# Kernel tuning notes

Measured on AMD Instinct MI355X. Metric: run time of the kernel, lower is better.

The kernel has to match this reference:

```python
import jax, jax.numpy as jnp
import numpy as np

N_NODES = 50000
N_EDGES = 800000
H = 128
LN_EPS = 1e-5


def setup_inputs() -> dict:
    key = jax.random.key(0)
    ks = jax.random.split(key, 8)
    x = jax.random.normal(ks[0], (N_NODES, H), dtype=jnp.float32)
    senders = jax.random.randint(ks[1], (N_EDGES,), 0, N_NODES, dtype=jnp.int32)
    receivers = jax.random.randint(ks[2], (N_EDGES,), 0, N_NODES, dtype=jnp.int32)
    edge_feat = jax.random.normal(ks[3], (N_EDGES, H), dtype=jnp.float32)
    # message_proj1: Linear(3H, H) -- PyTorch-style init scale
    lim = 1.0 / np.sqrt(3 * H)
    W1 = jax.random.uniform(ks[4], (3 * H, H), minval=-lim, maxval=lim, dtype=jnp.float32)
    b1 = jax.random.uniform(ks[5], (H,), minval=-lim, maxval=lim, dtype=jnp.float32)
    ln_gamma = jnp.ones((H,), dtype=jnp.float32)
    ln_beta = jnp.zeros((H,), dtype=jnp.float32)
    return {"x": x, "senders": senders, "receivers": receivers, "edge_feat": edge_feat,
            "W1": W1, "b1": b1, "ln_gamma": ln_gamma, "ln_beta": ln_beta}


def _layernorm(h, gamma, beta):
    mu = jnp.mean(h, axis=-1, keepdims=True)
    var = jnp.mean(jnp.square(h - mu), axis=-1, keepdims=True)
    return gamma * (h - mu) * jax.lax.rsqrt(var + LN_EPS) + beta


def reference(x, senders, receivers, edge_feat, W1, b1, ln_gamma, ln_beta):
    # gather sender/receiver node states, concat with edge features: [E, 3H]
    cat = jnp.concatenate((x[senders], x[receivers], edge_feat), axis=-1)
    msg = jax.nn.relu(cat @ W1 + b1)                      # [E, H]
    aggr = jax.ops.segment_sum(msg, receivers, num_segments=x.shape[0])  # [N, H]
    h = aggr + x                                          # residual
    return _layernorm(h, ln_gamma, ln_beta)
```

## Files before the change

### kernel.cpp

```cpp
#include <hip/hip_runtime.h>

#define NN 50000
#define NE 800000
#define H 128
#define K3H 384

typedef __bf16 bf16x8 __attribute__((ext_vector_type(8)));
typedef float f32x4 __attribute__((ext_vector_type(4)));

__device__ inline unsigned short f2bf(float f) {
    unsigned int u = __float_as_uint(f);
    u += 0x7FFFu + ((u >> 16) & 1u);
    return (unsigned short)(u >> 16);
}

__global__ void zero_aggr(float4* aggr) {
    int i = blockIdx.x * blockDim.x + threadIdx.x;
    aggr[i] = make_float4(0.f, 0.f, 0.f, 0.f);
}

__global__ void w1_transpose(const float* __restrict__ W1, unsigned short* __restrict__ W1t) {
    int o = blockIdx.x * 256 + threadIdx.x;
    if (o < K3H * H) {
        int n = o / K3H;
        int k = o - n * K3H;
        W1t[o] = f2bf(W1[k * H + n]);
    }
}

__global__ __launch_bounds__(256) void edge_gemm(
        const float* __restrict__ x,
        const int* __restrict__ senders,
        const int* __restrict__ receivers,
        const float* __restrict__ edge_feat,
        const unsigned short* __restrict__ W1t,
        const float* __restrict__ b1,
        float* __restrict__ aggr) {
    __shared__ short lds_a[128 * 72];
    __shared__ short lds_b[128 * 72];
    __shared__ int s_send[128];
    __shared__ int s_recv[128];

    const int tid = threadIdx.x;
    const int e0 = blockIdx.x * 128;

    if (tid < 128) s_send[tid] = senders[e0 + tid];
    else           s_recv[tid - 128] = receivers[e0 + tid - 128];
    __syncthreads();

    const int lane = tid & 63;
    const int wave = tid >> 6;
    const int wm = wave >> 1, wn = wave & 1;
    const int q = lane >> 4, l15 = lane & 15;

    f32x4 acc[4][4];
#pragma unroll
    for (int i = 0; i < 4; i++)
#pragma unroll
        for (int j = 0; j < 4; j++) acc[i][j] = (f32x4){0.f, 0.f, 0.f, 0.f};

    const int a_seg  = tid & 15;
    const int a_row0 = tid >> 4;
    const int b_seg  = tid & 7;
    const int b_row0 = tid >> 3;

    for (int c = 0; c < 6; ++c) {
        const int coloff = (c & 1) * 64;
#pragma unroll
        for (int p = 0; p < 8; ++p) {
            int row = a_row0 + p * 16;
            const float* src;
            if (c < 2)      src = x + (size_t)s_send[row] * H + coloff;
            else if (c < 4) src = x + (size_t)s_recv[row] * H + coloff;
            else            src = edge_feat + (size_t)(e0 + row) * H + coloff;
            float4 v = *(const float4*)(src + a_seg * 4);
            uint2 pk;
            pk.x = (unsigned)f2bf(v.x) | ((unsigned)f2bf(v.y) << 16);
            pk.y = (unsigned)f2bf(v.z) | ((unsigned)f2bf(v.w) << 16);
            *(uint2*)&lds_a[row * 72 + a_seg * 4] = pk;
        }
#pragma unroll
        for (int p = 0; p < 4; ++p) {
            int n = b_row0 + p * 32;
            uint4 v = *(const uint4*)(W1t + n * K3H + c * 64 + b_seg * 8);
            *(uint4*)&lds_b[n * 72 + b_seg * 8] = v;
        }
        __syncthreads();

        const short* pa = lds_a + (wm * 64 + l15) * 72 + q * 8;
        const short* pb = lds_b + (wn * 64 + l15) * 72 + q * 8;
#pragma unroll
        for (int ks = 0; ks < 2; ++ks) {
            bf16x8 af[4], bfr[4];
#pragma unroll
            for (int mi = 0; mi < 4; mi++)
                af[mi] = *(const bf16x8*)(const void*)(pa + mi * 16 * 72 + ks * 32);
#pragma unroll
            for (int ni = 0; ni < 4; ni++)
                bfr[ni] = *(const bf16x8*)(const void*)(pb + ni * 16 * 72 + ks * 32);
#pragma unroll
            for (int mi = 0; mi < 4; mi++)
#pragma unroll
                for (int ni = 0; ni < 4; ni++)
                    acc[mi][ni] = __builtin_amdgcn_mfma_f32_16x16x32_bf16(
                        af[mi], bfr[ni], acc[mi][ni], 0, 0, 0);
        }
        __syncthreads();
    }

    float bias[4];
#pragma unroll
    for (int ni = 0; ni < 4; ni++) bias[ni] = b1[wn * 64 + ni * 16 + l15];

#pragma unroll
    for (int mi = 0; mi < 4; mi++) {
        int rbase = wm * 64 + mi * 16 + q * 4;
#pragma unroll
        for (int r = 0; r < 4; r++) {
            int rl = rbase + r;
            int recv = s_recv[rl];
            float* dst = aggr + (size_t)recv * H + wn * 64 + l15;
#pragma unroll
            for (int ni = 0; ni < 4; ni++) {
                float v = acc[mi][ni][r] + bias[ni];
                if (v > 0.f) atomicAdd(dst + ni * 16, v);
            }
        }
    }
}

__global__ void residual_ln(const float* __restrict__ aggr, const float* __restrict__ x,
                            const float* __restrict__ gamma, const float* __restrict__ beta,
                            float* __restrict__ out) {
    int node = blockIdx.x * 4 + (threadIdx.x >> 6);
    int lane = threadIdx.x & 63;
    size_t off = (size_t)node * H + lane * 2;
    float2 a  = *(const float2*)(aggr + off);
    float2 xv = *(const float2*)(x + off);
    float h0 = a.x + xv.x, h1 = a.y + xv.y;
    float s = h0 + h1, sq = h0 * h0 + h1 * h1;
#pragma unroll
    for (int o = 32; o > 0; o >>= 1) {
        s  += __shfl_xor(s, o);
        sq += __shfl_xor(sq, o);
    }
    float mu  = s * (1.f / 128.f);
    float var = sq * (1.f / 128.f) - mu * mu;
    float rstd = rsqrtf(var + 1e-5f);
    float2 o2;
    o2.x = gamma[lane * 2]     * (h0 - mu) * rstd + beta[lane * 2];
    o2.y = gamma[lane * 2 + 1] * (h1 - mu) * rstd + beta[lane * 2 + 1];
    *(float2*)(out + off) = o2;
}

extern "C" void kernel_launch(void* const* d_in, const int* in_sizes, int n_in,
                              void* d_out, int out_size, void* d_ws, size_t ws_size,
                              hipStream_t stream) {
    const float* x         = (const float*)d_in[0];
    const int*   senders   = (const int*)d_in[1];
    const int*   receivers = (const int*)d_in[2];
    const float* edge_feat = (const float*)d_in[3];
    const float* W1        = (const float*)d_in[4];
    const float* b1        = (const float*)d_in[5];
    const float* gamma     = (const float*)d_in[6];
    const float* beta      = (const float*)d_in[7];
    float* out  = (float*)d_out;
    float* aggr = (float*)d_ws;
    unsigned short* W1t = (unsigned short*)((char*)d_ws + (size_t)NN * H * 4);

    zero_aggr<<<NN * H / 4 / 256, 256, 0, stream>>>((float4*)aggr);
    w1_transpose<<<(K3H * H + 255) / 256, 256, 0, stream>>>(W1, W1t);
    edge_gemm<<<NE / 128, 256, 0, stream>>>(x, senders, receivers, edge_feat, W1t, b1, aggr);
    residual_ln<<<NN / 4, 256, 0, stream>>>(aggr, x, gamma, beta, out);
}
```

Before: 848.0 us.

## Sort edges by receiver and segment-reduce messages before atomic adds

New measurement: 891.5 us. +5.1%, slower.

```diff
diff --git a/kernel.cpp b/kernel.cpp
--- a/kernel.cpp
+++ b/kernel.cpp
@@ -4,6 +4,7 @@
 #define NE 800000
 #define H 128
 #define K3H 384
+#define NBLK 196
 
 typedef __bf16 bf16x8 __attribute__((ext_vector_type(8)));
 typedef float f32x4 __attribute__((ext_vector_type(4)));
@@ -13,19 +14,77 @@
     u += 0x7FFFu + ((u >> 16) & 1u);
     return (unsigned short)(u >> 16);
 }
-
-__global__ void zero_aggr(float4* aggr) {
-    int i = blockIdx.x * blockDim.x + threadIdx.x;
-    aggr[i] = make_float4(0.f, 0.f, 0.f, 0.f);
-}
-
-__global__ void w1_transpose(const float* __restrict__ W1, unsigned short* __restrict__ W1t) {
+__device__ inline float bf2f(unsigned short u) {
+    return __uint_as_float(((unsigned)u) << 16);
+}
+
+__global__ void prep(const float* __restrict__ W1, unsigned short* __restrict__ W1t,
+                     int* __restrict__ count) {
     int o = blockIdx.x * 256 + threadIdx.x;
     if (o < K3H * H) {
         int n = o / K3H;
         int k = o - n * K3H;
         W1t[o] = f2bf(W1[k * H + n]);
     }
+    int c = o - K3H * H;
+    if (c >= 0 && c < NN) count[c] = 0;
+}
+
+__global__ void hist(const int* __restrict__ receivers, int* __restrict__ count) {
+    int e = blockIdx.x * 256 + threadIdx.x;
+    if (e < NE) atomicAdd(&count[receivers[e]], 1);
+}
+
+__global__ void scan_a(const int* __restrict__ count, int* __restrict__ offs,
+                       int* __restrict__ bsum) {
+    __shared__ int s[256];
+    int t = threadIdx.x, i = blockIdx.x * 256 + t;
+    int v = (i < NN) ? count[i] : 0;
+    s[t] = v; __syncthreads();
+    for (int off = 1; off < 256; off <<= 1) {
+        int u = (t >= off) ? s[t - off] : 0;
+        __syncthreads();
+        s[t] += u; __syncthreads();
+    }
+    if (i < NN) offs[i] = s[t] - v;
+    if (t == 255) bsum[blockIdx.x] = s[255];
+}
+
+__global__ void scan_b(int* __restrict__ bsum) {
+    __shared__ int s[256];
+    int t = threadIdx.x;
+    int v = (t < NBLK) ? bsum[t] : 0;
+    s[t] = v; __syncthreads();
+    for (int off = 1; off < 256; off <<= 1) {
+        int u = (t >= off) ? s[t - off] : 0;
+        __syncthreads();
+        s[t] += u; __syncthreads();
+    }
+    if (t < NBLK) bsum[t] = s[t] - v;
+}
+
+__global__ void scan_c(int* __restrict__ offs, const int* __restrict__ bsum,
+                       int* __restrict__ cursor) {
+    int i = blockIdx.x * 256 + threadIdx.x;
+    if (i < NN) {
+        int o = offs[i] + bsum[i >> 8];
+        offs[i] = o;
+        cursor[i] = o;
+    }
+}
+
+__global__ void scatter(const int* __restrict__ receivers, int* __restrict__ cursor,
+                        int* __restrict__ edge_of) {
+    int e = blockIdx.x * 256 + threadIdx.x;
+    if (e < NE) {
+        int pos = atomicAdd(&cursor[receivers[e]], 1);
+        edge_of[pos] = e;
+    }
+}
+
+__global__ void zero_aggr(float4* aggr) {
+    int i = blockIdx.x * blockDim.x + threadIdx.x;
+    aggr[i] = make_float4(0.f, 0.f, 0.f, 0.f);
 }
 
 __global__ __launch_bounds__(256) void edge_gemm(
@@ -35,17 +94,25 @@
         const float* __restrict__ edge_feat,
         const unsigned short* __restrict__ W1t,
         const float* __restrict__ b1,
+        const int* __restrict__ edge_of,
         float* __restrict__ aggr) {
-    __shared__ short lds_a[128 * 72];
-    __shared__ short lds_b[128 * 72];
+    __shared__ short smem[18432];
+    short* const lds_a = smem;
+    short* const lds_b = smem + 9216;
+    short* const lds_c = smem;
     __shared__ int s_send[128];
     __shared__ int s_recv[128];
+    __shared__ int s_eid[128];
 
     const int tid = threadIdx.x;
     const int e0 = blockIdx.x * 128;
 
-    if (tid < 128) s_send[tid] = senders[e0 + tid];
-    else           s_recv[tid - 128] = receivers[e0 + tid - 128];
+    if (tid < 128) {
+        int eid = edge_of[e0 + tid];
+        s_eid[tid]  = eid;
+        s_send[tid] = senders[eid];
+        s_recv[tid] = receivers[eid];
+    }
     __syncthreads();
 
     const int lane = tid & 63;
@@ -72,7 +139,7 @@
             const float* src;
             if (c < 2)      src = x + (size_t)s_send[row] * H + coloff;
             else if (c < 4) src = x + (size_t)s_recv[row] * H + coloff;
-            else            src = edge_feat + (size_t)(e0 + row) * H + coloff;
+            else            src = edge_feat + (size_t)s_eid[row] * H + coloff;
             float4 v = *(const float4*)(src + a_seg * 4);
             uint2 pk;
             pk.x = (unsigned)f2bf(v.x) | ((unsigned)f2bf(v.y) << 16);
@@ -116,16 +183,38 @@
     for (int mi = 0; mi < 4; mi++) {
         int rbase = wm * 64 + mi * 16 + q * 4;
 #pragma unroll
-        for (int r = 0; r < 4; r++) {
-            int rl = rbase + r;
-            int recv = s_recv[rl];
-            float* dst = aggr + (size_t)recv * H + wn * 64 + l15;
-#pragma unroll
-            for (int ni = 0; ni < 4; ni++) {
-                float v = acc[mi][ni][r] + bias[ni];
-                if (v > 0.f) atomicAdd(dst + ni * 16, v);
-            }
-        }
+        for (int ni = 0; ni < 4; ni++) {
+            int col = wn * 64 + ni * 16 + l15;
+            float v0 = acc[mi][ni][0] + bias[ni]; v0 = v0 > 0.f ? v0 : 0.f;
+            float v1 = acc[mi][ni][1] + bias[ni]; v1 = v1 > 0.f ? v1 : 0.f;
+            float v2 = acc[mi][ni][2] + bias[ni]; v2 = v2 > 0.f ? v2 : 0.f;
+            float v3 = acc[mi][ni][3] + bias[ni]; v3 = v3 > 0.f ? v3 : 0.f;
+            uint2 pk;
+            pk.x = (unsigned)f2bf(v0) | ((unsigned)f2bf(v1) << 16);
+            pk.y = (unsigned)f2bf(v2) | ((unsigned)f2bf(v3) << 16);
+            *(uint2*)&lds_c[col * 132 + rbase] = pk;
+        }
+    }
+    __syncthreads();
+
+    {
+        const int col  = tid & 127;
+        const int half = tid >> 7;
+        const int r0 = half * 64;
+        const short* pc = lds_c + col * 132;
+        int prev = s_recv[r0];
+        float sum = 0.f;
+#pragma unroll 8
+        for (int row = r0; row < r0 + 64; row += 2) {
+            unsigned pk = *(const unsigned*)(pc + row);
+            int rc0 = s_recv[row];
+            int rc1 = s_recv[row + 1];
+            if (rc0 != prev) { atomicAdd(&aggr[(size_t)prev * H + col], sum); sum = 0.f; prev = rc0; }
+            sum += bf2f((unsigned short)(pk & 0xFFFFu));
+            if (rc1 != prev) { atomicAdd(&aggr[(size_t)prev * H + col], sum); sum = 0.f; prev = rc1; }
+            sum += bf2f((unsigned short)(pk >> 16));
+        }
+        atomicAdd(&aggr[(size_t)prev * H + col], sum);
     }
 }
 
@@ -164,12 +253,25 @@
     const float* b1        = (const float*)d_in[5];
     const float* gamma     = (const float*)d_in[6];
     const float* beta      = (const float*)d_in[7];
-    float* out  = (float*)d_out;
-    float* aggr = (float*)d_ws;
-    unsigned short* W1t = (unsigned short*)((char*)d_ws + (size_t)NN * H * 4);
-
+    float* out = (float*)d_out;
+
+    char* ws = (char*)d_ws;
+    float*          aggr    = (float*)(ws);
+    unsigned short* W1t     = (unsigned short*)(ws + 25600000);
+    int*            count   = (int*)(ws + 25698304);
+    int*            offs    = (int*)(ws + 25898304);
+    int*            cursor  = (int*)(ws + 26098304);
+    int*            bsum    = (int*)(ws + 26298304);
+    int*            edge_of = (int*)(ws + 26299328);
+
+    prep<<<388, 256, 0, stream>>>(W1, W1t, count);
+    hist<<<NE / 256, 256, 0, stream>>>(receivers, count);
+    scan_a<<<NBLK, 256, 0, stream>>>(count, offs, bsum);
+    scan_b<<<1, 256, 0, stream>>>(bsum);
+    scan_c<<<NBLK, 256, 0, stream>>>(offs, bsum, cursor);
+    scatter<<<NE / 256, 256, 0, stream>>>(receivers, cursor, edge_of);
     zero_aggr<<<NN * H / 4 / 256, 256, 0, stream>>>((float4*)aggr);
-    w1_transpose<<<(K3H * H + 255) / 256, 256, 0, stream>>>(W1, W1t);
-    edge_gemm<<<NE / 128, 256, 0, stream>>>(x, senders, receivers, edge_feat, W1t, b1, aggr);
+    edge_gemm<<<NE / 128, 256, 0, stream>>>(x, senders, receivers, edge_feat, W1t, b1,
+                                            edge_of, aggr);
     residual_ln<<<NN / 4, 256, 0, stream>>>(aggr, x, gamma, beta, out);
 }
```
